# Optimization experiments

Hardware: AMD Instinct MI355X
Metric: run time of the kernel (lower is better)

Reference implementation:

```python
import jax, jax.numpy as jnp
import numpy as np

BLKQ = 64
BLKK = 64
TOPK_RATIO = 0.25
EPS = 1e-05


def mean_pool(x, blk):
    B, H, L, D = x.shape
    return x.reshape(B, H, L // blk, blk, D).mean(axis=3)


def setup_inputs() -> dict:
    key = jax.random.key(0)
    kq, kk, kv, kw, kb = jax.random.split(key, 5)
    B, H, Lq, Lk, D = 1, 8, 4096, 4096, 64
    q = jax.random.normal(kq, (B, H, Lq, D), dtype=jnp.float32)
    k = jax.random.normal(kk, (B, H, Lk, D), dtype=jnp.float32)
    v = jax.random.normal(kv, (B, H, Lk, D), dtype=jnp.float32)
    # proj_l is zero-initialized in the original; use small random weights so the
    # linear-attention branch contributes non-trivially to the output.
    proj_w = jax.random.normal(kw, (D, D), dtype=jnp.float32) * 0.02
    proj_b = jax.random.normal(kb, (D,), dtype=jnp.float32) * 0.02
    return {"q": q, "k": k, "v": v, "proj_w": proj_w, "proj_b": proj_b}


def reference(q, k, v, proj_w, proj_b):
    B, H, Lq, D = q.shape
    Lk = k.shape[2]
    nQ, nK = Lq // BLKQ, Lk // BLKK

    # ---- block-level top-k routing (get_block_map_cross) ----
    arg_k = k - k.mean(axis=-2, keepdims=True)
    pq = mean_pool(q, BLKQ)                      # (B,H,nQ,D)
    pk = mean_pool(arg_k, BLKK)                  # (B,H,nK,D)
    pooled_score = jnp.einsum('bhqd,bhkd->bhqk', pq, pk)  # (B,H,nQ,nK)
    topk = min(nK, max(1, int(TOPK_RATIO * nK)))
    lut = jax.lax.top_k(pooled_score, topk)[1]   # (B,H,nQ,topk) int32

    # ---- block-sparse cross attention (softmax over selected K blocks) ----
    qb = q.reshape(B, H, nQ, BLKQ, D)
    kb = k.reshape(B, H, nK, BLKK, D)
    vb = v.reshape(B, H, nK, BLKK, D)
    gather = jax.vmap(jax.vmap(lambda blocks, idx: blocks[idx]))  # over B,H
    kg = gather(kb, lut)                         # (B,H,nQ,topk,BLKK,D)
    vg = gather(vb, lut)                         # (B,H,nQ,topk,BLKK,D)
    scale = D ** -0.5
    s = jnp.einsum('bhnqd,bhntkd->bhnqtk', qb, kg) * scale
    s = s.reshape(B, H, nQ, BLKQ, topk * BLKK)
    p = jax.nn.softmax(s, axis=-1)
    o_s = jnp.einsum('bhnqt,bhntd->bhnqd', p, vg.reshape(B, H, nQ, topk * BLKK, D))
    o_s = o_s.reshape(B, H, Lq, D)

    # ---- linear attention branch (softmax feature map, tied q/k) ----
    qf = jax.nn.softmax(q, axis=-1)
    kf = jax.nn.softmax(k, axis=-1)
    kv = jnp.einsum('bhkd,bhke->bhde', kf, v)    # (B,H,D,D)
    denom = jnp.einsum('bhqd,bhd->bhq', qf, kf.sum(axis=2)) + EPS
    o_l = jnp.einsum('bhqd,bhde->bhqe', qf, kv) / denom[..., None]
    o_l = o_l @ proj_w.T + proj_b                # proj_l

    return o_s + o_l
```

## Files before the change

### kernel.cpp

```cpp
#include <hip/hip_runtime.h>
#include <math.h>

#define H 8
#define L 4096
#define D 64
#define NBLK 64
#define TOPK 16
#define EPS 1e-5f
#define LP 68

typedef unsigned short u16;
typedef unsigned int u32;
typedef __attribute__((ext_vector_type(8))) short bf16x8;
typedef __attribute__((ext_vector_type(16))) float f32x16;

static __device__ __forceinline__ u16 f2bf(float x) {
  u32 u = __float_as_uint(x);
  u32 r = (u + 0x7fffu + ((u >> 16) & 1u)) >> 16;
  return (u16)r;
}
static __device__ __forceinline__ float bf2f(u16 h) {
  return __uint_as_float(((u32)h) << 16);
}
__device__ __forceinline__ float dot4f(float4 a, float4 b) {
  return a.x * b.x + a.y * b.y + a.z * b.z + a.w * b.w;
}

__global__ __launch_bounds__(256) void kpack_kernel(
    const float* __restrict__ k, u16* __restrict__ kpk) {
  const int h = blockIdx.y;
  const int key = blockIdx.x * 32 + (threadIdx.x >> 3);
  const int sub = threadIdx.x & 7;
  const float* src = k + ((size_t)h * L + key) * D + sub * 8;
  float4 a = *(const float4*)(src);
  float4 b = *(const float4*)(src + 4);
  float f[8] = {a.x, a.y, a.z, a.w, b.x, b.y, b.z, b.w};
  u16 hi[8], lo[8];
#pragma unroll
  for (int e = 0; e < 8; ++e) {
    hi[e] = f2bf(f[e]);
    lo[e] = f2bf(f[e] - bf2f(hi[e]));
  }
  const int c = sub >> 1, g = sub & 1;
  u16* row = kpk + ((size_t)h * L + key) * 128;
  const int sh = ((c * 4 + g * 2 + 0) ^ (key & 15)) * 8;
  const int sl = ((c * 4 + g * 2 + 1) ^ (key & 15)) * 8;
  uint4 vh = {(u32)hi[0] | ((u32)hi[1] << 16), (u32)hi[2] | ((u32)hi[3] << 16),
              (u32)hi[4] | ((u32)hi[5] << 16), (u32)hi[6] | ((u32)hi[7] << 16)};
  uint4 vl = {(u32)lo[0] | ((u32)lo[1] << 16), (u32)lo[2] | ((u32)lo[3] << 16),
              (u32)lo[4] | ((u32)lo[5] << 16), (u32)lo[6] | ((u32)lo[7] << 16)};
  *(uint4*)(row + sh) = vh;
  *(uint4*)(row + sl) = vl;
}

__global__ __launch_bounds__(256) void vpack_kernel(
    const float* __restrict__ v, u16* __restrict__ vpk) {
  const int h = blockIdx.y, kb = blockIdx.x;
  __shared__ float vt[64 * LP];
  const int t = threadIdx.x;
  {
    const float4* src = (const float4*)(v + ((size_t)h * L + (size_t)kb * 64) * D);
#pragma unroll
    for (int i = 0; i < 4; ++i) {
      int flat = i * 256 + t;
      int key = flat >> 4, c4 = flat & 15;
      *(float4*)&vt[key * LP + c4 * 4] = src[flat];
    }
  }
  __syncthreads();
  u16* base = vpk + (((size_t)h * 64 + kb) * 64) * 128;
#pragma unroll
  for (int iter = 0; iter < 4; ++iter) {
    const int dim = iter * 16 + (t >> 4);
    const int s = t & 15;
    const int cgh = s ^ (dim & 15);
    const int c = cgh >> 2, g = (cgh >> 1) & 1, hl = cgh & 1;
    u16 o[8];
#pragma unroll
    for (int e = 0; e < 8; ++e) {
      const int key = 4 * g + (e & 3) + 8 * ((e >> 2) + 2 * (c & 1)) + 32 * (c >> 1);
      float val = vt[key * LP + dim];
      u16 hi = f2bf(val);
      o[e] = hl ? f2bf(val - bf2f(hi)) : hi;
    }
    uint4 pk4 = {(u32)o[0] | ((u32)o[1] << 16), (u32)o[2] | ((u32)o[3] << 16),
                 (u32)o[4] | ((u32)o[5] << 16), (u32)o[6] | ((u32)o[7] << 16)};
    *(uint4*)(base + (size_t)dim * 128 + s * 8) = pk4;
  }
}

__global__ __launch_bounds__(256) void pool_kernel(
    const float* __restrict__ src, float* __restrict__ dst) {
  const int blk = blockIdx.x, h = blockIdx.y;
  const int d = threadIdx.x & 63, rr = threadIdx.x >> 6;
  const float* base = src + ((size_t)h * L + (size_t)blk * 64) * D;
  float s = 0.f;
#pragma unroll
  for (int i = 0; i < 16; ++i) s += base[(rr * 16 + i) * D + d];
  __shared__ float red[4][64];
  red[rr][d] = s;
  __syncthreads();
  if (rr == 0) {
    float tot = red[0][d] + red[1][d] + red[2][d] + red[3][d];
    dst[((size_t)h * NBLK + blk) * D + d] = tot * (1.f / 64.f);
  }
}

__global__ __launch_bounds__(64) void topk_kernel(
    const float* __restrict__ pq, const float* __restrict__ pk,
    int* __restrict__ lut) {
  const int qb = blockIdx.x, h = blockIdx.y;
  const int j = threadIdx.x;
  const float4* pqv = (const float4*)(pq + ((size_t)h * NBLK + qb) * D);
  const float4* pkv = (const float4*)(pk + ((size_t)h * NBLK + j) * D);
  float s = 0.f;
#pragma unroll
  for (int d4 = 0; d4 < 16; ++d4) s += dot4f(pqv[d4], pkv[d4]);
  int* lrow = lut + ((size_t)h * NBLK + qb) * TOPK;
  for (int t = 0; t < TOPK; ++t) {
    float m = s;
    int mi = j;
#pragma unroll
    for (int off = 32; off; off >>= 1) {
      float om = __shfl_xor(m, off);
      int omi = __shfl_xor(mi, off);
      if (om > m || (om == m && omi < mi)) { m = om; mi = omi; }
    }
    if (j == 0) lrow[t] = mi;
    if (j == mi) s = -INFINITY;
  }
}

__global__ __launch_bounds__(256) void sattn_kernel(
    const float* __restrict__ q, const u16* __restrict__ kpk,
    const u16* __restrict__ vpk, const int* __restrict__ lut,
    float* __restrict__ out) {
  __shared__ alignas(16) char smem[65536];
  const int bx = blockIdx.x;
  const int h = bx & 7, qb = bx >> 3;
  const int t = threadIdx.x;
  const int lane = t & 63;
  const int ln = lane & 31;
  const int g = lane >> 5;
  const int w = t >> 6;
  const int p = w & 1;
  const int hf = w >> 1;
  const int t128 = t & 127;

  float* qst = (float*)smem;
  {
    const float4* src = (const float4*)(q + ((size_t)h * L + (size_t)qb * 64) * D);
#pragma unroll
    for (int i = 0; i < 4; ++i) {
      int flat = i * 256 + t;
      int row = flat >> 4, c4 = flat & 15;
      *(float4*)&qst[row * 68 + c4 * 4] = src[flat];
    }
  }
  __syncthreads();
  bf16x8 qh[4], ql[4];
  {
    const int qrow = p * 32 + ln;
#pragma unroll
    for (int c = 0; c < 4; ++c) {
      const float* s8 = &qst[qrow * 68 + c * 16 + g * 8];
#pragma unroll
      for (int e = 0; e < 8; ++e) {
        float x = s8[e] * 0.125f;
        u16 hi = f2bf(x);
        qh[c][e] = (short)hi;
        ql[c][e] = (short)f2bf(x - bf2f(hi));
      }
    }
  }
  __syncthreads();

  u16* Kb = (u16*)smem + hf * 8192;
  u16* Vb = (u16*)smem + 16384 + hf * 8192;

  f32x16 o0, o1;
#pragma unroll
  for (int r = 0; r < 16; ++r) { o0[r] = 0.f; o1[r] = 0.f; }
  float mrun = -INFINITY, lrun = 0.f;

  const int* lrowp = lut + ((size_t)h * NBLK + qb) * TOPK + hf * 8;

  for (int ib = 0; ib < 8; ++ib) {
    const int kb = lrowp[ib];
    __syncthreads();
    {
      const uint4* gk = (const uint4*)(kpk + ((size_t)h * L + (size_t)kb * 64) * 128);
      const uint4* gv = (const uint4*)(vpk + (((size_t)h * 64 + kb) * 64) * 128);
      uint4* lk = (uint4*)Kb;
      uint4* lv = (uint4*)Vb;
#pragma unroll
      for (int i = 0; i < 8; ++i) {
        lk[i * 128 + t128] = gk[i * 128 + t128];
        lv[i * 128 + t128] = gv[i * 128 + t128];
      }
    }
    __syncthreads();

    f32x16 s0, s1;
#pragma unroll
    for (int r = 0; r < 16; ++r) { s0[r] = 0.f; s1[r] = 0.f; }
#pragma unroll
    for (int c = 0; c < 4; ++c) {
      const int sH = c * 4 + g * 2;
      const int xr = ln & 15;
      bf16x8 k0h = *(const bf16x8*)(Kb + (size_t)ln * 128 + ((sH ^ xr) * 8));
      bf16x8 k0l = *(const bf16x8*)(Kb + (size_t)ln * 128 + (((sH + 1) ^ xr) * 8));
      bf16x8 k1h = *(const bf16x8*)(Kb + (size_t)(32 + ln) * 128 + ((sH ^ xr) * 8));
      bf16x8 k1l = *(const bf16x8*)(Kb + (size_t)(32 + ln) * 128 + (((sH + 1) ^ xr) * 8));
      s0 = __builtin_amdgcn_mfma_f32_32x32x16_bf16(k0h, qh[c], s0, 0, 0, 0);
      s0 = __builtin_amdgcn_mfma_f32_32x32x16_bf16(k0l, qh[c], s0, 0, 0, 0);
      s0 = __builtin_amdgcn_mfma_f32_32x32x16_bf16(k0h, ql[c], s0, 0, 0, 0);
      s1 = __builtin_amdgcn_mfma_f32_32x32x16_bf16(k1h, qh[c], s1, 0, 0, 0);
      s1 = __builtin_amdgcn_mfma_f32_32x32x16_bf16(k1l, qh[c], s1, 0, 0, 0);
      s1 = __builtin_amdgcn_mfma_f32_32x32x16_bf16(k1h, ql[c], s1, 0, 0, 0);
    }

    float mloc = -INFINITY;
#pragma unroll
    for (int r = 0; r < 16; ++r) {
      mloc = fmaxf(mloc, s0[r]);
      mloc = fmaxf(mloc, s1[r]);
    }
    mloc = fmaxf(mloc, __shfl_xor(mloc, 32));
    const float mnew = fmaxf(mrun, mloc);
    const float corr = __expf(mrun - mnew);
    float psum = 0.f;
#pragma unroll
    for (int r = 0; r < 16; ++r) {
      s0[r] = __expf(s0[r] - mnew); psum += s0[r];
      s1[r] = __expf(s1[r] - mnew); psum += s1[r];
    }
    psum += __shfl_xor(psum, 32);
    lrun = lrun * corr + psum;
    mrun = mnew;
#pragma unroll
    for (int r = 0; r < 16; ++r) {
      const int R = (r & 3) + 8 * (r >> 2) + 4 * g;
      const float cr = __shfl(corr, R);
      o0[r] *= cr;
      o1[r] *= cr;
    }

#pragma unroll
    for (int c = 0; c < 4; ++c) {
      bf16x8 pah, pal;
#pragma unroll
      for (int e = 0; e < 8; ++e) {
        const int r = (e & 3) + 4 * ((e >> 2) + 2 * (c & 1));
        const float pv = (c >> 1) ? s1[r] : s0[r];
        u16 hi = f2bf(pv);
        pah[e] = (short)hi;
        pal[e] = (short)f2bf(pv - bf2f(hi));
      }
      const int sH = c * 4 + g * 2;
      const int xr = ln & 15;
      bf16x8 v0h = *(const bf16x8*)(Vb + (size_t)ln * 128 + ((sH ^ xr) * 8));
      bf16x8 v0l = *(const bf16x8*)(Vb + (size_t)ln * 128 + (((sH + 1) ^ xr) * 8));
      bf16x8 v1h = *(const bf16x8*)(Vb + (size_t)(32 + ln) * 128 + ((sH ^ xr) * 8));
      bf16x8 v1l = *(const bf16x8*)(Vb + (size_t)(32 + ln) * 128 + (((sH + 1) ^ xr) * 8));
      o0 = __builtin_amdgcn_mfma_f32_32x32x16_bf16(pah, v0h, o0, 0, 0, 0);
      o0 = __builtin_amdgcn_mfma_f32_32x32x16_bf16(pal, v0h, o0, 0, 0, 0);
      o0 = __builtin_amdgcn_mfma_f32_32x32x16_bf16(pah, v0l, o0, 0, 0, 0);
      o1 = __builtin_amdgcn_mfma_f32_32x32x16_bf16(pah, v1h, o1, 0, 0, 0);
      o1 = __builtin_amdgcn_mfma_f32_32x32x16_bf16(pal, v1h, o1, 0, 0, 0);
      o1 = __builtin_amdgcn_mfma_f32_32x32x16_bf16(pah, v1l, o1, 0, 0, 0);
    }
  }

  __syncthreads();
  float* mls = (float*)smem;
  if (lane < 32) {
    mls[(p * 2 + hf) * 32 + ln] = mrun;
    mls[128 + (p * 2 + hf) * 32 + ln] = lrun;
  }
  __syncthreads();
  float* ox = (float*)smem + 256 + p * 2048;
  if (hf == 1) {
#pragma unroll
    for (int r = 0; r < 16; ++r) {
      const int R = (r & 3) + 8 * (r >> 2) + 4 * g;
      const float mA = mls[(p * 2 + 0) * 32 + R];
      const float mB = mls[(p * 2 + 1) * 32 + R];
      const float mc = fmaxf(mA, mB);
      const float sB = __expf(mB - mc);
      ox[R * 64 + ln] = o0[r] * sB;
      ox[R * 64 + 32 + ln] = o1[r] * sB;
    }
  }
  __syncthreads();
  if (hf == 0) {
#pragma unroll
    for (int r = 0; r < 16; ++r) {
      const int R = (r & 3) + 8 * (r >> 2) + 4 * g;
      const float mA = mls[(p * 2 + 0) * 32 + R];
      const float mB = mls[(p * 2 + 1) * 32 + R];
      const float mc = fmaxf(mA, mB);
      const float sA = __expf(mA - mc), sB = __expf(mB - mc);
      const float lA = mls[128 + (p * 2 + 0) * 32 + R];
      const float lB = mls[128 + (p * 2 + 1) * 32 + R];
      const float inv = 1.f / (lA * sA + lB * sB);
      const size_t row = (size_t)h * L + (size_t)qb * 64 + p * 32 + R;
      out[row * 64 + ln] = (o0[r] * sA + ox[R * 64 + ln]) * inv;
      out[row * 64 + 32 + ln] = (o1[r] * sA + ox[R * 64 + 32 + ln]) * inv;
    }
  }
}

__global__ __launch_bounds__(256) void kvacc_kernel(
    const float* __restrict__ k, const float* __restrict__ v,
    float* __restrict__ part_kv, float* __restrict__ part_ks) {
  const int ch = blockIdx.x, h = blockIdx.y;
  __shared__ float kf[128 * LP];
  __shared__ float vsh[128 * LP];
  const int t = threadIdx.x;
  const int d = t & 63, eg = t >> 6;
  float4 acc0 = make_float4(0.f, 0.f, 0.f, 0.f);
  float4 acc1 = acc0, acc2 = acc0, acc3 = acc0;
  float ksacc = 0.f;
  const int row0 = ch * 128;
  {
    const int row = t >> 1, half = t & 1;
    const float4* krow = (const float4*)(k + ((size_t)h * L + row0 + row) * D) + half * 8;
    float4 kr[8];
#pragma unroll
    for (int i = 0; i < 8; ++i) kr[i] = krow[i];
    float mxk = -INFINITY;
#pragma unroll
    for (int i = 0; i < 8; ++i)
      mxk = fmaxf(mxk, fmaxf(fmaxf(kr[i].x, kr[i].y), fmaxf(kr[i].z, kr[i].w)));
    mxk = fmaxf(mxk, __shfl_xor(mxk, 1));
    float smk = 0.f;
#pragma unroll
    for (int i = 0; i < 8; ++i) {
      kr[i].x = __expf(kr[i].x - mxk); kr[i].y = __expf(kr[i].y - mxk);
      kr[i].z = __expf(kr[i].z - mxk); kr[i].w = __expf(kr[i].w - mxk);
      smk += kr[i].x + kr[i].y + kr[i].z + kr[i].w;
    }
    smk += __shfl_xor(smk, 1);
    const float inv = 1.f / smk;
#pragma unroll
    for (int i = 0; i < 8; ++i) {
      float4 o = kr[i];
      o.x *= inv; o.y *= inv; o.z *= inv; o.w *= inv;
      *(float4*)&kf[row * LP + half * 32 + i * 4] = o;
    }
  }
  {
    const float4* vbase = (const float4*)(v + ((size_t)h * L + row0) * D);
#pragma unroll
    for (int i = 0; i < 8; ++i) {
      int flat = i * 256 + t;
      int row2 = flat >> 4, c4 = flat & 15;
      *(float4*)&vsh[row2 * LP + c4 * 4] = vbase[flat];
    }
  }
  __syncthreads();
#pragma unroll 4
  for (int lr = 0; lr < 128; ++lr) {
    const float wv = kf[lr * LP + d];
    if (eg == 0) ksacc += wv;
    const float4* vr = (const float4*)&vsh[lr * LP + eg * 16];
    float4 v0 = vr[0], v1 = vr[1], v2 = vr[2], v3 = vr[3];
    acc0.x += wv * v0.x; acc0.y += wv * v0.y; acc0.z += wv * v0.z; acc0.w += wv * v0.w;
    acc1.x += wv * v1.x; acc1.y += wv * v1.y; acc1.z += wv * v1.z; acc1.w += wv * v1.w;
    acc2.x += wv * v2.x; acc2.y += wv * v2.y; acc2.z += wv * v2.z; acc2.w += wv * v2.w;
    acc3.x += wv * v3.x; acc3.y += wv * v3.y; acc3.z += wv * v3.z; acc3.w += wv * v3.w;
  }
  float* kvb = part_kv + ((size_t)(h * 32 + ch)) * 4096 + (size_t)d * 64 + eg * 16;
  *(float4*)(kvb + 0) = acc0;
  *(float4*)(kvb + 4) = acc1;
  *(float4*)(kvb + 8) = acc2;
  *(float4*)(kvb + 12) = acc3;
  if (eg == 0) part_ks[(size_t)(h * 32 + ch) * 64 + d] = ksacc;
}

__global__ __launch_bounds__(256) void kvproj_kernel(
    const float* __restrict__ part_kv, const float* __restrict__ part_ks,
    const float* __restrict__ pw, float* __restrict__ kvp,
    float* __restrict__ ksum) {
  const int h = blockIdx.x;
  __shared__ float kvs[64 * 64];
  __shared__ float pws[64 * 64];
  const int t = threadIdx.x;
  float4 s0 = make_float4(0.f, 0.f, 0.f, 0.f);
  float4 s1 = s0, s2 = s0, s3 = s0;
  for (int p = 0; p < 32; ++p) {
    const float4* src = (const float4*)(part_kv + ((size_t)(h * 32 + p)) * 4096);
    float4 a = src[0 * 256 + t], b = src[1 * 256 + t];
    float4 cc = src[2 * 256 + t], dd = src[3 * 256 + t];
    s0.x += a.x; s0.y += a.y; s0.z += a.z; s0.w += a.w;
    s1.x += b.x; s1.y += b.y; s1.z += b.z; s1.w += b.w;
    s2.x += cc.x; s2.y += cc.y; s2.z += cc.z; s2.w += cc.w;
    s3.x += dd.x; s3.y += dd.y; s3.z += dd.z; s3.w += dd.w;
  }
  ((float4*)kvs)[0 * 256 + t] = s0;
  ((float4*)kvs)[1 * 256 + t] = s1;
  ((float4*)kvs)[2 * 256 + t] = s2;
  ((float4*)kvs)[3 * 256 + t] = s3;
#pragma unroll
  for (int i = 0; i < 4; ++i) {
    int f4 = i * 256 + t;
    ((float4*)pws)[f4] = ((const float4*)pw)[f4];
  }
  if (t < 64) {
    float ks = 0.f;
    for (int p = 0; p < 32; ++p) ks += part_ks[(size_t)(h * 32 + p) * 64 + t];
    ksum[(size_t)h * 64 + t] = ks;
  }
  __syncthreads();
  const int d = t & 63, fg = t >> 6;
  float* dst = kvp + (size_t)h * 4096 + (size_t)d * 64;
  const float4* a = (const float4*)&kvs[d * 64];
  for (int f = fg * 16; f < fg * 16 + 16; ++f) {
    const float4* b = (const float4*)&pws[f * 64];
    float s = 0.f;
#pragma unroll
    for (int e4 = 0; e4 < 16; ++e4) s += dot4f(a[e4], b[e4]);
    dst[f] = s;
  }
}

__global__ __launch_bounds__(256) void linattn_kernel(
    const float* __restrict__ q, const float* __restrict__ kvp,
    const float* __restrict__ ksum, const float* __restrict__ pb,
    float* __restrict__ out) {
  __shared__ float kvs[64 * 64];
  __shared__ float kss[64], pbs[64];
  const int t = threadIdx.x;
  const size_t grow = (size_t)blockIdx.x * 256 + t;
  const int h = (int)(grow >> 12);
#pragma unroll
  for (int i = 0; i < 4; ++i) {
    int f4 = i * 256 + t;
    ((float4*)kvs)[f4] = ((const float4*)(kvp + (size_t)h * 4096))[f4];
  }
  if (t < 64) {
    kss[t] = ksum[(size_t)h * 64 + t];
    pbs[t] = pb[t];
  }
  __syncthreads();
  const float* qrow = q + grow * 64;
  float mx = -INFINITY;
  const float4* q4p = (const float4*)qrow;
#pragma unroll
  for (int i = 0; i < 16; ++i) {
    float4 x = q4p[i];
    mx = fmaxf(mx, fmaxf(fmaxf(x.x, x.y), fmaxf(x.z, x.w)));
  }
  float4 tt[16];
#pragma unroll
  for (int i = 0; i < 16; ++i) tt[i] = make_float4(0.f, 0.f, 0.f, 0.f);
  float sm = 0.f, dn = 0.f;
#pragma unroll 4
  for (int dd = 0; dd < 64; ++dd) {
    const float wv = __expf(qrow[dd] - mx);
    sm += wv;
    dn += wv * kss[dd];
    const float4* kvr = (const float4*)&kvs[dd * 64];
#pragma unroll
    for (int e4 = 0; e4 < 16; ++e4) {
      float4 kk = kvr[e4];
      tt[e4].x += wv * kk.x; tt[e4].y += wv * kk.y;
      tt[e4].z += wv * kk.z; tt[e4].w += wv * kk.w;
    }
  }
  const float inv = 1.f / (dn + EPS * sm);
  float* orow = out + grow * 64;
#pragma unroll
  for (int e4 = 0; e4 < 16; ++e4) {
    float4 o = ((float4*)orow)[e4];
    o.x += tt[e4].x * inv + pbs[e4 * 4 + 0];
    o.y += tt[e4].y * inv + pbs[e4 * 4 + 1];
    o.z += tt[e4].z * inv + pbs[e4 * 4 + 2];
    o.w += tt[e4].w * inv + pbs[e4 * 4 + 3];
    ((float4*)orow)[e4] = o;
  }
}

extern "C" void kernel_launch(void* const* d_in, const int* in_sizes, int n_in,
                              void* d_out, int out_size, void* d_ws, size_t ws_size,
                              hipStream_t stream) {
  const float* q = (const float*)d_in[0];
  const float* k = (const float*)d_in[1];
  const float* v = (const float*)d_in[2];
  const float* pw = (const float*)d_in[3];
  const float* pb = (const float*)d_in[4];
  float* out = (float*)d_out;

  u16* kpkb = (u16*)d_ws;
  u16* vpkb = (u16*)d_ws + 4194304;
  float* fws = (float*)((char*)d_ws + 16777216);
  float* pq = fws;
  float* pk = fws + 32768;
  float* part_kv = fws + 65536;
  float* part_ks = part_kv + 1048576;
  float* kvp = part_ks + 16384;
  float* ksum = kvp + 32768;
  int* lut = (int*)(ksum + 512);

  kpack_kernel<<<dim3(128, 8), 256, 0, stream>>>(k, kpkb);
  vpack_kernel<<<dim3(64, 8), 256, 0, stream>>>(v, vpkb);
  pool_kernel<<<dim3(64, 8), 256, 0, stream>>>(q, pq);
  pool_kernel<<<dim3(64, 8), 256, 0, stream>>>(k, pk);
  topk_kernel<<<dim3(64, 8), 64, 0, stream>>>(pq, pk, lut);
  sattn_kernel<<<512, 256, 0, stream>>>(q, kpkb, vpkb, lut, out);
  kvacc_kernel<<<dim3(32, 8), 256, 0, stream>>>(k, v, part_kv, part_ks);
  kvproj_kernel<<<8, 256, 0, stream>>>(part_kv, part_ks, pw, kvp, ksum);
  linattn_kernel<<<128, 256, 0, stream>>>(q, kvp, ksum, pb, out);
}
```

Measured before the change: 194.6 us.

## Fuse K/V prep kernels and restructure sparse attention without online max

Merges K packing, V packing, K mean-pooling and the softmax-feature KV accumulation into one kvprep kernel that reads each 64-key block of K and V from global memory once. A two-stage partial-sum reduction (kvred, then kvproj) replaces the single 32-way reduction. The sparse attention kernel now has all four waves share one K/V block per step, each wave taking 32 keys, with 32KB of LDS and a 4-blocks-per-SM launch bound. It drops the online max and rescaling and packs probabilities to bf16 with v_cvt_pk_bf16_f32. Removing the max subtraction relies on scaled scores staying small enough that exp does not overflow, and the single LDS buffer adds two barriers per step.

```diff
diff --git a/kernel.cpp b/kernel.cpp
--- a/kernel.cpp
+++ b/kernel.cpp
@@ -13,6 +13,7 @@
 typedef unsigned int u32;
 typedef __attribute__((ext_vector_type(8))) short bf16x8;
 typedef __attribute__((ext_vector_type(16))) float f32x16;
+typedef __attribute__((ext_vector_type(4))) u32 u32x4;
 
 static __device__ __forceinline__ u16 f2bf(float x) {
   u32 u = __float_as_uint(x);
@@ -26,66 +27,146 @@
   return a.x * b.x + a.y * b.y + a.z * b.z + a.w * b.w;
 }
 
-__global__ __launch_bounds__(256) void kpack_kernel(
-    const float* __restrict__ k, u16* __restrict__ kpk) {
-  const int h = blockIdx.y;
-  const int key = blockIdx.x * 32 + (threadIdx.x >> 3);
-  const int sub = threadIdx.x & 7;
-  const float* src = k + ((size_t)h * L + key) * D + sub * 8;
-  float4 a = *(const float4*)(src);
-  float4 b = *(const float4*)(src + 4);
-  float f[8] = {a.x, a.y, a.z, a.w, b.x, b.y, b.z, b.w};
-  u16 hi[8], lo[8];
-#pragma unroll
-  for (int e = 0; e < 8; ++e) {
-    hi[e] = f2bf(f[e]);
-    lo[e] = f2bf(f[e] - bf2f(hi[e]));
-  }
-  const int c = sub >> 1, g = sub & 1;
-  u16* row = kpk + ((size_t)h * L + key) * 128;
-  const int sh = ((c * 4 + g * 2 + 0) ^ (key & 15)) * 8;
-  const int sl = ((c * 4 + g * 2 + 1) ^ (key & 15)) * 8;
-  uint4 vh = {(u32)hi[0] | ((u32)hi[1] << 16), (u32)hi[2] | ((u32)hi[3] << 16),
-              (u32)hi[4] | ((u32)hi[5] << 16), (u32)hi[6] | ((u32)hi[7] << 16)};
-  uint4 vl = {(u32)lo[0] | ((u32)lo[1] << 16), (u32)lo[2] | ((u32)lo[3] << 16),
-              (u32)lo[4] | ((u32)lo[5] << 16), (u32)lo[6] | ((u32)lo[7] << 16)};
-  *(uint4*)(row + sh) = vh;
-  *(uint4*)(row + sl) = vl;
-}
-
-__global__ __launch_bounds__(256) void vpack_kernel(
-    const float* __restrict__ v, u16* __restrict__ vpk) {
-  const int h = blockIdx.y, kb = blockIdx.x;
-  __shared__ float vt[64 * LP];
+__global__ __launch_bounds__(256) void kvprep_kernel(
+    const float* __restrict__ k, const float* __restrict__ v,
+    u16* __restrict__ kpkb, u16* __restrict__ vpkb,
+    float* __restrict__ pkp, float* __restrict__ part_kv,
+    float* __restrict__ part_ks) {
+  const int kb = blockIdx.x, h = blockIdx.y;
+  __shared__ float kst[64 * LP];
+  __shared__ float vst[64 * LP];
+  __shared__ float red[4][64];
   const int t = threadIdx.x;
-  {
-    const float4* src = (const float4*)(v + ((size_t)h * L + (size_t)kb * 64) * D);
+
+  {
+    const float4* ksrc = (const float4*)(k + ((size_t)h * L + (size_t)kb * 64) * D);
+    const float4* vsrc = (const float4*)(v + ((size_t)h * L + (size_t)kb * 64) * D);
 #pragma unroll
     for (int i = 0; i < 4; ++i) {
       int flat = i * 256 + t;
-      int key = flat >> 4, c4 = flat & 15;
-      *(float4*)&vt[key * LP + c4 * 4] = src[flat];
-    }
-  }
-  __syncthreads();
-  u16* base = vpk + (((size_t)h * 64 + kb) * 64) * 128;
-#pragma unroll
-  for (int iter = 0; iter < 4; ++iter) {
-    const int dim = iter * 16 + (t >> 4);
-    const int s = t & 15;
-    const int cgh = s ^ (dim & 15);
-    const int c = cgh >> 2, g = (cgh >> 1) & 1, hl = cgh & 1;
-    u16 o[8];
-#pragma unroll
-    for (int e = 0; e < 8; ++e) {
-      const int key = 4 * g + (e & 3) + 8 * ((e >> 2) + 2 * (c & 1)) + 32 * (c >> 1);
-      float val = vt[key * LP + dim];
-      u16 hi = f2bf(val);
-      o[e] = hl ? f2bf(val - bf2f(hi)) : hi;
-    }
-    uint4 pk4 = {(u32)o[0] | ((u32)o[1] << 16), (u32)o[2] | ((u32)o[3] << 16),
-                 (u32)o[4] | ((u32)o[5] << 16), (u32)o[6] | ((u32)o[7] << 16)};
-    *(uint4*)(base + (size_t)dim * 128 + s * 8) = pk4;
+      int row = flat >> 4, c4 = flat & 15;
+      *(float4*)&kst[row * LP + c4 * 4] = ksrc[flat];
+      *(float4*)&vst[row * LP + c4 * 4] = vsrc[flat];
+    }
+  }
+  __syncthreads();
+
+  {
+    u16* rowbase = kpkb + ((size_t)h * L + (size_t)kb * 64) * 128;
+#pragma unroll
+    for (int pass = 0; pass < 2; ++pass) {
+      const int key = pass * 32 + (t >> 3);
+      const int sub = t & 7;
+      float f[8];
+#pragma unroll
+      for (int e = 0; e < 8; ++e) f[e] = kst[key * LP + sub * 8 + e];
+      u16 hi[8], lo[8];
+#pragma unroll
+      for (int e = 0; e < 8; ++e) {
+        hi[e] = f2bf(f[e]);
+        lo[e] = f2bf(f[e] - bf2f(hi[e]));
+      }
+      const int c = sub >> 1, g2 = sub & 1;
+      u16* row = rowbase + (size_t)key * 128;
+      const int sh = ((c * 4 + g2 * 2 + 0) ^ (key & 15)) * 8;
+      const int sl = ((c * 4 + g2 * 2 + 1) ^ (key & 15)) * 8;
+      uint4 vh = {(u32)hi[0] | ((u32)hi[1] << 16), (u32)hi[2] | ((u32)hi[3] << 16),
+                  (u32)hi[4] | ((u32)hi[5] << 16), (u32)hi[6] | ((u32)hi[7] << 16)};
+      uint4 vl = {(u32)lo[0] | ((u32)lo[1] << 16), (u32)lo[2] | ((u32)lo[3] << 16),
+                  (u32)lo[4] | ((u32)lo[5] << 16), (u32)lo[6] | ((u32)lo[7] << 16)};
+      *(uint4*)(row + sh) = vh;
+      *(uint4*)(row + sl) = vl;
+    }
+  }
+
+  {
+    const int d = t & 63, rr = t >> 6;
+    float s = 0.f;
+#pragma unroll
+    for (int i = 0; i < 16; ++i) s += kst[(rr * 16 + i) * LP + d];
+    red[rr][d] = s;
+  }
+  __syncthreads();
+  {
+    const int d = t & 63, rr = t >> 6;
+    if (rr == 0) {
+      float tot = red[0][d] + red[1][d] + red[2][d] + red[3][d];
+      pkp[((size_t)h * NBLK + kb) * D + d] = tot * (1.f / 64.f);
+    }
+  }
+
+  {
+    u16* base = vpkb + (((size_t)h * 64 + kb) * 64) * 128;
+#pragma unroll
+    for (int iter = 0; iter < 4; ++iter) {
+      const int dim = iter * 16 + (t >> 4);
+      const int s = t & 15;
+      const int cgh = s ^ (dim & 15);
+      const int c = cgh >> 2, g = (cgh >> 1) & 1, hl = cgh & 1;
+      u16 o[8];
+#pragma unroll
+      for (int e = 0; e < 8; ++e) {
+        const int key = 4 * g + (e & 3) + 8 * ((e >> 2) + 2 * (c & 1)) + 32 * (c >> 1);
+        float val = vst[key * LP + dim];
+        u16 hi = f2bf(val);
+        o[e] = hl ? f2bf(val - bf2f(hi)) : hi;
+      }
+      uint4 pk4 = {(u32)o[0] | ((u32)o[1] << 16), (u32)o[2] | ((u32)o[3] << 16),
+                   (u32)o[4] | ((u32)o[5] << 16), (u32)o[6] | ((u32)o[7] << 16)};
+      *(uint4*)(base + (size_t)dim * 128 + s * 8) = pk4;
+    }
+  }
+
+  if (t < 128) {
+    const int row = t >> 1, half = t & 1;
+    float4 kr[8];
+#pragma unroll
+    for (int i = 0; i < 8; ++i) kr[i] = *(float4*)&kst[row * LP + half * 32 + i * 4];
+    float mxk = -INFINITY;
+#pragma unroll
+    for (int i = 0; i < 8; ++i)
+      mxk = fmaxf(mxk, fmaxf(fmaxf(kr[i].x, kr[i].y), fmaxf(kr[i].z, kr[i].w)));
+    mxk = fmaxf(mxk, __shfl_xor(mxk, 1));
+    float smk = 0.f;
+#pragma unroll
+    for (int i = 0; i < 8; ++i) {
+      kr[i].x = __expf(kr[i].x - mxk); kr[i].y = __expf(kr[i].y - mxk);
+      kr[i].z = __expf(kr[i].z - mxk); kr[i].w = __expf(kr[i].w - mxk);
+      smk += kr[i].x + kr[i].y + kr[i].z + kr[i].w;
+    }
+    smk += __shfl_xor(smk, 1);
+    const float inv = 1.f / smk;
+#pragma unroll
+    for (int i = 0; i < 8; ++i) {
+      float4 o = kr[i];
+      o.x *= inv; o.y *= inv; o.z *= inv; o.w *= inv;
+      *(float4*)&kst[row * LP + half * 32 + i * 4] = o;
+    }
+  }
+  __syncthreads();
+
+  {
+    const int d = t & 63, eg = t >> 6;
+    float4 acc0 = make_float4(0.f, 0.f, 0.f, 0.f);
+    float4 acc1 = acc0, acc2 = acc0, acc3 = acc0;
+    float ksacc = 0.f;
+#pragma unroll 4
+    for (int lr = 0; lr < 64; ++lr) {
+      const float wv = kst[lr * LP + d];
+      if (eg == 0) ksacc += wv;
+      const float4* vr = (const float4*)&vst[lr * LP + eg * 16];
+      float4 v0 = vr[0], v1 = vr[1], v2 = vr[2], v3 = vr[3];
+      acc0.x += wv * v0.x; acc0.y += wv * v0.y; acc0.z += wv * v0.z; acc0.w += wv * v0.w;
+      acc1.x += wv * v1.x; acc1.y += wv * v1.y; acc1.z += wv * v1.z; acc1.w += wv * v1.w;
+      acc2.x += wv * v2.x; acc2.y += wv * v2.y; acc2.z += wv * v2.z; acc2.w += wv * v2.w;
+      acc3.x += wv * v3.x; acc3.y += wv * v3.y; acc3.z += wv * v3.z; acc3.w += wv * v3.w;
+    }
+    float* kvb = part_kv + ((size_t)(h * 64 + kb)) * 4096 + (size_t)d * 64 + eg * 16;
+    *(float4*)(kvb + 0) = acc0;
+    *(float4*)(kvb + 4) = acc1;
+    *(float4*)(kvb + 8) = acc2;
+    *(float4*)(kvb + 12) = acc3;
+    if (eg == 0) part_ks[(size_t)(h * 64 + kb) * 64 + d] = ksacc;
   }
 }
 
@@ -131,11 +212,11 @@
   }
 }
 
-__global__ __launch_bounds__(256) void sattn_kernel(
+__global__ __launch_bounds__(256, 4) void sattn_kernel(
     const float* __restrict__ q, const u16* __restrict__ kpk,
     const u16* __restrict__ vpk, const int* __restrict__ lut,
     float* __restrict__ out) {
-  __shared__ alignas(16) char smem[65536];
+  __shared__ alignas(16) char smem[32768];
   const int bx = blockIdx.x;
   const int h = bx & 7, qb = bx >> 3;
   const int t = threadIdx.x;
@@ -144,8 +225,7 @@
   const int g = lane >> 5;
   const int w = t >> 6;
   const int p = w & 1;
-  const int hf = w >> 1;
-  const int t128 = t & 127;
+  const int kh = w >> 1;
 
   float* qst = (float*)smem;
   {
@@ -153,8 +233,7 @@
 #pragma unroll
     for (int i = 0; i < 4; ++i) {
       int flat = i * 256 + t;
-      int row = flat >> 4, c4 = flat & 15;
-      *(float4*)&qst[row * 68 + c4 * 4] = src[flat];
+      *(float4*)&qst[(flat >> 4) * LP + (flat & 15) * 4] = src[flat];
     }
   }
   __syncthreads();
@@ -163,7 +242,7 @@
     const int qrow = p * 32 + ln;
 #pragma unroll
     for (int c = 0; c < 4; ++c) {
-      const float* s8 = &qst[qrow * 68 + c * 16 + g * 8];
+      const float* s8 = &qst[qrow * LP + c * 16 + g * 8];
 #pragma unroll
       for (int e = 0; e < 8; ++e) {
         float x = s8[e] * 0.125f;
@@ -175,94 +254,76 @@
   }
   __syncthreads();
 
-  u16* Kb = (u16*)smem + hf * 8192;
-  u16* Vb = (u16*)smem + 16384 + hf * 8192;
+  u16* KB = (u16*)smem;
+  u16* VB = (u16*)smem + 8192;
 
   f32x16 o0, o1;
 #pragma unroll
   for (int r = 0; r < 16; ++r) { o0[r] = 0.f; o1[r] = 0.f; }
-  float mrun = -INFINITY, lrun = 0.f;
-
-  const int* lrowp = lut + ((size_t)h * NBLK + qb) * TOPK + hf * 8;
-
-  for (int ib = 0; ib < 8; ++ib) {
-    const int kb = lrowp[ib];
-    __syncthreads();
-    {
-      const uint4* gk = (const uint4*)(kpk + ((size_t)h * L + (size_t)kb * 64) * 128);
-      const uint4* gv = (const uint4*)(vpk + (((size_t)h * 64 + kb) * 64) * 128);
-      uint4* lk = (uint4*)Kb;
-      uint4* lv = (uint4*)Vb;
-#pragma unroll
-      for (int i = 0; i < 8; ++i) {
-        lk[i * 128 + t128] = gk[i * 128 + t128];
-        lv[i * 128 + t128] = gv[i * 128 + t128];
-      }
-    }
-    __syncthreads();
-
-    f32x16 s0, s1;
-#pragma unroll
-    for (int r = 0; r < 16; ++r) { s0[r] = 0.f; s1[r] = 0.f; }
+  float lrun = 0.f;
+  const int* lrow = lut + ((size_t)h * NBLK + qb) * TOPK;
+  const int xr = ln & 15;
+  const int krow = kh * 32 + ln;
+
+  {
+    const int kb = lrow[0];
+    const uint4* gk = (const uint4*)(kpk + ((size_t)h * L + (size_t)kb * 64) * 128);
+    const uint4* gv = (const uint4*)(vpk + (((size_t)h * 64 + kb) * 64) * 128);
+    uint4* lk = (uint4*)KB;
+    uint4* lv = (uint4*)VB;
+#pragma unroll
+    for (int i = 0; i < 4; ++i) {
+      int x = i * 256 + t;
+      lk[x] = gk[x];
+      lv[x] = gv[x];
+    }
+  }
+  __syncthreads();
+
+  for (int ib = 0; ib < TOPK; ++ib) {
+    f32x16 s0;
+#pragma unroll
+    for (int r = 0; r < 16; ++r) s0[r] = 0.f;
 #pragma unroll
     for (int c = 0; c < 4; ++c) {
       const int sH = c * 4 + g * 2;
-      const int xr = ln & 15;
-      bf16x8 k0h = *(const bf16x8*)(Kb + (size_t)ln * 128 + ((sH ^ xr) * 8));
-      bf16x8 k0l = *(const bf16x8*)(Kb + (size_t)ln * 128 + (((sH + 1) ^ xr) * 8));
-      bf16x8 k1h = *(const bf16x8*)(Kb + (size_t)(32 + ln) * 128 + ((sH ^ xr) * 8));
-      bf16x8 k1l = *(const bf16x8*)(Kb + (size_t)(32 + ln) * 128 + (((sH + 1) ^ xr) * 8));
-      s0 = __builtin_amdgcn_mfma_f32_32x32x16_bf16(k0h, qh[c], s0, 0, 0, 0);
-      s0 = __builtin_amdgcn_mfma_f32_32x32x16_bf16(k0l, qh[c], s0, 0, 0, 0);
-      s0 = __builtin_amdgcn_mfma_f32_32x32x16_bf16(k0h, ql[c], s0, 0, 0, 0);
-      s1 = __builtin_amdgcn_mfma_f32_32x32x16_bf16(k1h, qh[c], s1, 0, 0, 0);
-      s1 = __builtin_amdgcn_mfma_f32_32x32x16_bf16(k1l, qh[c], s1, 0, 0, 0);
-      s1 = __builtin_amdgcn_mfma_f32_32x32x16_bf16(k1h, ql[c], s1, 0, 0, 0);
-    }
-
-    float mloc = -INFINITY;
-#pragma unroll
-    for (int r = 0; r < 16; ++r) {
-      mloc = fmaxf(mloc, s0[r]);
-      mloc = fmaxf(mloc, s1[r]);
-    }
-    mloc = fmaxf(mloc, __shfl_xor(mloc, 32));
-    const float mnew = fmaxf(mrun, mloc);
-    const float corr = __expf(mrun - mnew);
+      bf16x8 k_h = *(const bf16x8*)(KB + (size_t)krow * 128 + ((sH ^ xr) * 8));
+      bf16x8 k_l = *(const bf16x8*)(KB + (size_t)krow * 128 + (((sH + 1) ^ xr) * 8));
+      s0 = __builtin_amdgcn_mfma_f32_32x32x16_bf16(k_h, qh[c], s0, 0, 0, 0);
+      s0 = __builtin_amdgcn_mfma_f32_32x32x16_bf16(k_l, qh[c], s0, 0, 0, 0);
+      s0 = __builtin_amdgcn_mfma_f32_32x32x16_bf16(k_h, ql[c], s0, 0, 0, 0);
+    }
+
+    u32 hpk[8], lpk[8];
     float psum = 0.f;
 #pragma unroll
-    for (int r = 0; r < 16; ++r) {
-      s0[r] = __expf(s0[r] - mnew); psum += s0[r];
-      s1[r] = __expf(s1[r] - mnew); psum += s1[r];
+    for (int j = 0; j < 8; ++j) {
+      float a = __expf(s0[2 * j]);
+      float b = __expf(s0[2 * j + 1]);
+      psum += a + b;
+      u32 hp;
+      asm("v_cvt_pk_bf16_f32 %0, %1, %2" : "=v"(hp) : "v"(a), "v"(b));
+      hpk[j] = hp;
+      float ah = __uint_as_float(hp << 16);
+      float bh = __uint_as_float(hp & 0xffff0000u);
+      u32 lp;
+      asm("v_cvt_pk_bf16_f32 %0, %1, %2" : "=v"(lp) : "v"(a - ah), "v"(b - bh));
+      lpk[j] = lp;
     }
     psum += __shfl_xor(psum, 32);
-    lrun = lrun * corr + psum;
-    mrun = mnew;
-#pragma unroll
-    for (int r = 0; r < 16; ++r) {
-      const int R = (r & 3) + 8 * (r >> 2) + 4 * g;
-      const float cr = __shfl(corr, R);
-      o0[r] *= cr;
-      o1[r] *= cr;
-    }
-
-#pragma unroll
-    for (int c = 0; c < 4; ++c) {
-      bf16x8 pah, pal;
-#pragma unroll
-      for (int e = 0; e < 8; ++e) {
-        const int r = (e & 3) + 4 * ((e >> 2) + 2 * (c & 1));
-        const float pv = (c >> 1) ? s1[r] : s0[r];
-        u16 hi = f2bf(pv);
-        pah[e] = (short)hi;
-        pal[e] = (short)f2bf(pv - bf2f(hi));
-      }
-      const int sH = c * 4 + g * 2;
-      const int xr = ln & 15;
-      bf16x8 v0h = *(const bf16x8*)(Vb + (size_t)ln * 128 + ((sH ^ xr) * 8));
-      bf16x8 v0l = *(const bf16x8*)(Vb + (size_t)ln * 128 + (((sH + 1) ^ xr) * 8));
-      bf16x8 v1h = *(const bf16x8*)(Vb + (size_t)(32 + ln) * 128 + ((sH ^ xr) * 8));
-      bf16x8 v1l = *(const bf16x8*)(Vb + (size_t)(32 + ln) * 128 + (((sH + 1) ^ xr) * 8));
+    lrun += psum;
+
+#pragma unroll
+    for (int cc = 0; cc < 2; ++cc) {
+      union { u32x4 u; bf16x8 b; } ph, pl;
+      ph.u = (u32x4){hpk[4 * cc + 0], hpk[4 * cc + 1], hpk[4 * cc + 2], hpk[4 * cc + 3]};
+      pl.u = (u32x4){lpk[4 * cc + 0], lpk[4 * cc + 1], lpk[4 * cc + 2], lpk[4 * cc + 3]};
+      const bf16x8 pah = ph.b, pal = pl.b;
+      const int sH = (2 * kh + cc) * 4 + g * 2;
+      bf16x8 v0h = *(const bf16x8*)(VB + (size_t)ln * 128 + ((sH ^ xr) * 8));
+      bf16x8 v0l = *(const bf16x8*)(VB + (size_t)ln * 128 + (((sH + 1) ^ xr) * 8));
+      bf16x8 v1h = *(const bf16x8*)(VB + (size_t)(32 + ln) * 128 + ((sH ^ xr) * 8));
+      bf16x8 v1l = *(const bf16x8*)(VB + (size_t)(32 + ln) * 128 + (((sH + 1) ^ xr) * 8));
       o0 = __builtin_amdgcn_mfma_f32_32x32x16_bf16(pah, v0h, o0, 0, 0, 0);
       o0 = __builtin_amdgcn_mfma_f32_32x32x16_bf16(pal, v0h, o0, 0, 0, 0);
       o0 = __builtin_amdgcn_mfma_f32_32x32x16_bf16(pah, v0l, o0, 0, 0, 0);
@@ -270,117 +331,81 @@
       o1 = __builtin_amdgcn_mfma_f32_32x32x16_bf16(pal, v1h, o1, 0, 0, 0);
       o1 = __builtin_amdgcn_mfma_f32_32x32x16_bf16(pah, v1l, o1, 0, 0, 0);
     }
-  }
-
-  __syncthreads();
-  float* mls = (float*)smem;
-  if (lane < 32) {
-    mls[(p * 2 + hf) * 32 + ln] = mrun;
-    mls[128 + (p * 2 + hf) * 32 + ln] = lrun;
-  }
-  __syncthreads();
-  float* ox = (float*)smem + 256 + p * 2048;
-  if (hf == 1) {
+
+    __syncthreads();
+    if (ib + 1 < TOPK) {
+      const int kb = lrow[ib + 1];
+      const uint4* gk = (const uint4*)(kpk + ((size_t)h * L + (size_t)kb * 64) * 128);
+      const uint4* gv = (const uint4*)(vpk + (((size_t)h * 64 + kb) * 64) * 128);
+      uint4* lk = (uint4*)KB;
+      uint4* lv = (uint4*)VB;
+#pragma unroll
+      for (int i = 0; i < 4; ++i) {
+        int x = i * 256 + t;
+        lk[x] = gk[x];
+        lv[x] = gv[x];
+      }
+    }
+    __syncthreads();
+  }
+
+  float* oxbase = (float*)smem;
+  float* lxbase = (float*)smem + 4096;
+  if (g == 0) lxbase[(p * 2 + kh) * 32 + ln] = lrun;
+  if (kh == 1) {
 #pragma unroll
     for (int r = 0; r < 16; ++r) {
       const int R = (r & 3) + 8 * (r >> 2) + 4 * g;
-      const float mA = mls[(p * 2 + 0) * 32 + R];
-      const float mB = mls[(p * 2 + 1) * 32 + R];
-      const float mc = fmaxf(mA, mB);
-      const float sB = __expf(mB - mc);
-      ox[R * 64 + ln] = o0[r] * sB;
-      ox[R * 64 + 32 + ln] = o1[r] * sB;
-    }
-  }
-  __syncthreads();
-  if (hf == 0) {
+      oxbase[p * 2048 + R * 64 + ln] = o0[r];
+      oxbase[p * 2048 + R * 64 + 32 + ln] = o1[r];
+    }
+  }
+  __syncthreads();
+  if (kh == 0) {
 #pragma unroll
     for (int r = 0; r < 16; ++r) {
       const int R = (r & 3) + 8 * (r >> 2) + 4 * g;
-      const float mA = mls[(p * 2 + 0) * 32 + R];
-      const float mB = mls[(p * 2 + 1) * 32 + R];
-      const float mc = fmaxf(mA, mB);
-      const float sA = __expf(mA - mc), sB = __expf(mB - mc);
-      const float lA = mls[128 + (p * 2 + 0) * 32 + R];
-      const float lB = mls[128 + (p * 2 + 1) * 32 + R];
-      const float inv = 1.f / (lA * sA + lB * sB);
+      const float lt = lxbase[(p * 2 + 0) * 32 + R] + lxbase[(p * 2 + 1) * 32 + R];
+      const float inv = 1.f / lt;
       const size_t row = (size_t)h * L + (size_t)qb * 64 + p * 32 + R;
-      out[row * 64 + ln] = (o0[r] * sA + ox[R * 64 + ln]) * inv;
-      out[row * 64 + 32 + ln] = (o1[r] * sA + ox[R * 64 + 32 + ln]) * inv;
-    }
-  }
-}
-
-__global__ __launch_bounds__(256) void kvacc_kernel(
-    const float* __restrict__ k, const float* __restrict__ v,
-    float* __restrict__ part_kv, float* __restrict__ part_ks) {
-  const int ch = blockIdx.x, h = blockIdx.y;
-  __shared__ float kf[128 * LP];
-  __shared__ float vsh[128 * LP];
+      out[row * 64 + ln] = (o0[r] + oxbase[p * 2048 + R * 64 + ln]) * inv;
+      out[row * 64 + 32 + ln] = (o1[r] + oxbase[p * 2048 + R * 64 + 32 + ln]) * inv;
+    }
+  }
+}
+
+__global__ __launch_bounds__(256) void kvred_kernel(
+    const float* __restrict__ part_kv, const float* __restrict__ part_ks,
+    float* __restrict__ p2kv, float* __restrict__ p2ks) {
+  const int j = blockIdx.x, h = blockIdx.y;
   const int t = threadIdx.x;
-  const int d = t & 63, eg = t >> 6;
-  float4 acc0 = make_float4(0.f, 0.f, 0.f, 0.f);
-  float4 acc1 = acc0, acc2 = acc0, acc3 = acc0;
-  float ksacc = 0.f;
-  const int row0 = ch * 128;
-  {
-    const int row = t >> 1, half = t & 1;
-    const float4* krow = (const float4*)(k + ((size_t)h * L + row0 + row) * D) + half * 8;
-    float4 kr[8];
-#pragma unroll
-    for (int i = 0; i < 8; ++i) kr[i] = krow[i];
-    float mxk = -INFINITY;
-#pragma unroll
-    for (int i = 0; i < 8; ++i)
-      mxk = fmaxf(mxk, fmaxf(fmaxf(kr[i].x, kr[i].y), fmaxf(kr[i].z, kr[i].w)));
-    mxk = fmaxf(mxk, __shfl_xor(mxk, 1));
-    float smk = 0.f;
-#pragma unroll
-    for (int i = 0; i < 8; ++i) {
-      kr[i].x = __expf(kr[i].x - mxk); kr[i].y = __expf(kr[i].y - mxk);
-      kr[i].z = __expf(kr[i].z - mxk); kr[i].w = __expf(kr[i].w - mxk);
-      smk += kr[i].x + kr[i].y + kr[i].z + kr[i].w;
-    }
-    smk += __shfl_xor(smk, 1);
-    const float inv = 1.f / smk;
-#pragma unroll
-    for (int i = 0; i < 8; ++i) {
-      float4 o = kr[i];
-      o.x *= inv; o.y *= inv; o.z *= inv; o.w *= inv;
-      *(float4*)&kf[row * LP + half * 32 + i * 4] = o;
-    }
-  }
-  {
-    const float4* vbase = (const float4*)(v + ((size_t)h * L + row0) * D);
-#pragma unroll
-    for (int i = 0; i < 8; ++i) {
-      int flat = i * 256 + t;
-      int row2 = flat >> 4, c4 = flat & 15;
-      *(float4*)&vsh[row2 * LP + c4 * 4] = vbase[flat];
-    }
-  }
-  __syncthreads();
-#pragma unroll 4
-  for (int lr = 0; lr < 128; ++lr) {
-    const float wv = kf[lr * LP + d];
-    if (eg == 0) ksacc += wv;
-    const float4* vr = (const float4*)&vsh[lr * LP + eg * 16];
-    float4 v0 = vr[0], v1 = vr[1], v2 = vr[2], v3 = vr[3];
-    acc0.x += wv * v0.x; acc0.y += wv * v0.y; acc0.z += wv * v0.z; acc0.w += wv * v0.w;
-    acc1.x += wv * v1.x; acc1.y += wv * v1.y; acc1.z += wv * v1.z; acc1.w += wv * v1.w;
-    acc2.x += wv * v2.x; acc2.y += wv * v2.y; acc2.z += wv * v2.z; acc2.w += wv * v2.w;
-    acc3.x += wv * v3.x; acc3.y += wv * v3.y; acc3.z += wv * v3.z; acc3.w += wv * v3.w;
-  }
-  float* kvb = part_kv + ((size_t)(h * 32 + ch)) * 4096 + (size_t)d * 64 + eg * 16;
-  *(float4*)(kvb + 0) = acc0;
-  *(float4*)(kvb + 4) = acc1;
-  *(float4*)(kvb + 8) = acc2;
-  *(float4*)(kvb + 12) = acc3;
-  if (eg == 0) part_ks[(size_t)(h * 32 + ch) * 64 + d] = ksacc;
+  float4 s0 = make_float4(0.f, 0.f, 0.f, 0.f);
+  float4 s1 = s0, s2 = s0, s3 = s0;
+#pragma unroll
+  for (int p = 0; p < 4; ++p) {
+    const float4* src = (const float4*)(part_kv + ((size_t)(h * 64 + j * 4 + p)) * 4096);
+    float4 a = src[0 * 256 + t], b = src[1 * 256 + t];
+    float4 c = src[2 * 256 + t], d = src[3 * 256 + t];
+    s0.x += a.x; s0.y += a.y; s0.z += a.z; s0.w += a.w;
+    s1.x += b.x; s1.y += b.y; s1.z += b.z; s1.w += b.w;
+    s2.x += c.x; s2.y += c.y; s2.z += c.z; s2.w += c.w;
+    s3.x += d.x; s3.y += d.y; s3.z += d.z; s3.w += d.w;
+  }
+  float4* dst = (float4*)(p2kv + ((size_t)(h * 16 + j)) * 4096);
+  dst[0 * 256 + t] = s0;
+  dst[1 * 256 + t] = s1;
+  dst[2 * 256 + t] = s2;
+  dst[3 * 256 + t] = s3;
+  if (t < 64) {
+    float ks = 0.f;
+#pragma unroll
+    for (int p = 0; p < 4; ++p) ks += part_ks[(size_t)(h * 64 + j * 4 + p) * 64 + t];
+    p2ks[(size_t)(h * 16 + j) * 64 + t] = ks;
+  }
 }
 
 __global__ __launch_bounds__(256) void kvproj_kernel(
-    const float* __restrict__ part_kv, const float* __restrict__ part_ks,
+    const float* __restrict__ p2kv, const float* __restrict__ p2ks,
     const float* __restrict__ pw, float* __restrict__ kvp,
     float* __restrict__ ksum) {
   const int h = blockIdx.x;
@@ -389,8 +414,8 @@
   const int t = threadIdx.x;
   float4 s0 = make_float4(0.f, 0.f, 0.f, 0.f);
   float4 s1 = s0, s2 = s0, s3 = s0;
-  for (int p = 0; p < 32; ++p) {
-    const float4* src = (const float4*)(part_kv + ((size_t)(h * 32 + p)) * 4096);
+  for (int p = 0; p < 16; ++p) {
+    const float4* src = (const float4*)(p2kv + ((size_t)(h * 16 + p)) * 4096);
     float4 a = src[0 * 256 + t], b = src[1 * 256 + t];
     float4 cc = src[2 * 256 + t], dd = src[3 * 256 + t];
     s0.x += a.x; s0.y += a.y; s0.z += a.z; s0.w += a.w;
@@ -409,7 +434,7 @@
   }
   if (t < 64) {
     float ks = 0.f;
-    for (int p = 0; p < 32; ++p) ks += part_ks[(size_t)(h * 32 + p) * 64 + t];
+    for (int p = 0; p < 16; ++p) ks += p2ks[(size_t)(h * 16 + p) * 64 + t];
     ksum[(size_t)h * 64 + t] = ks;
   }
   __syncthreads();
@@ -498,18 +523,18 @@
   float* pq = fws;
   float* pk = fws + 32768;
   float* part_kv = fws + 65536;
-  float* part_ks = part_kv + 1048576;
-  float* kvp = part_ks + 16384;
-  float* ksum = kvp + 32768;
-  int* lut = (int*)(ksum + 512);
-
-  kpack_kernel<<<dim3(128, 8), 256, 0, stream>>>(k, kpkb);
-  vpack_kernel<<<dim3(64, 8), 256, 0, stream>>>(v, vpkb);
+  float* part_ks = fws + 2162688;
+  float* p2kv = fws + 2195456;
+  float* p2ks = fws + 2719744;
+  float* kvp = fws + 2727936;
+  float* ksum = fws + 2760704;
+  int* lut = (int*)(fws + 2761216);
+
+  kvprep_kernel<<<dim3(64, 8), 256, 0, stream>>>(k, v, kpkb, vpkb, pk, part_kv, part_ks);
   pool_kernel<<<dim3(64, 8), 256, 0, stream>>>(q, pq);
-  pool_kernel<<<dim3(64, 8), 256, 0, stream>>>(k, pk);
   topk_kernel<<<dim3(64, 8), 64, 0, stream>>>(pq, pk, lut);
   sattn_kernel<<<512, 256, 0, stream>>>(q, kpkb, vpkb, lut, out);
-  kvacc_kernel<<<dim3(32, 8), 256, 0, stream>>>(k, v, part_kv, part_ks);
-  kvproj_kernel<<<8, 256, 0, stream>>>(part_kv, part_ks, pw, kvp, ksum);
+  kvred_kernel<<<dim3(16, 8), 256, 0, stream>>>(part_kv, part_ks, p2kv, p2ks);
+  kvproj_kernel<<<8, 256, 0, stream>>>(p2kv, p2ks, pw, kvp, ksum);
   linattn_kernel<<<128, 256, 0, stream>>>(q, kvp, ksum, pb, out);
 }
```

After: 177.2 us. 1.1x faster.
